# Kernel optimization log

Measured on AMD Instinct MI355X. Metric: run time of the kernel, lower is better.

The kernel has to match this reference:

```python
import jax, jax.numpy as jnp
import numpy as np

N_VERTEX = 50000
N_EDGE = 400000
HV, HE, P, Q, MV, ME = 128, 64, 3, 3, 128, 128


def setup_inputs() -> dict:
    key = jax.random.key(0)
    ks = jax.random.split(key, 12)
    hv_ftr = jax.random.normal(ks[0], (N_VERTEX, HV), jnp.float32)
    he_ftr = jax.random.normal(ks[1], (N_EDGE, HE), jnp.float32)
    p_ftr = jax.random.normal(ks[2], (N_VERTEX, P), jnp.float32)
    q_ftr = jax.random.normal(ks[3], (N_VERTEX, Q), jnp.float32)
    edge_u = jax.random.randint(ks[4], (N_EDGE,), 0, N_VERTEX, jnp.int32)
    edge_v = jax.random.randint(ks[5], (N_EDGE,), 0, N_VERTEX, jnp.int32)
    # Linear params stored as [in, out] (y = x @ W + b), matching torch Linear math.
    Wa = jax.random.normal(ks[6], (HV, MV), jnp.float32) * 0.05      # attend
    ba = jnp.zeros((MV,), jnp.float32)
    Wal = jax.random.normal(ks[7], (P + Q + HE, 1), jnp.float32) * 0.05  # align
    bal = jnp.zeros((1,), jnp.float32)
    Wl = jax.random.normal(ks[8], (2 * HV + P + Q, ME), jnp.float32) * 0.05  # link
    bl = jnp.zeros((ME,), jnp.float32)
    return dict(hv_ftr=hv_ftr, he_ftr=he_ftr, p_ftr=p_ftr, q_ftr=q_ftr,
                edge_u=edge_u, edge_v=edge_v,
                Wa=Wa, ba=ba, Wal=Wal, bal=bal, Wl=Wl, bl=bl)


def reference(hv_ftr, he_ftr, p_ftr, q_ftr, edge_u, edge_v, Wa, ba, Wal, bal, Wl, bl):
    # dropout is p=0.0 (identity). The dense vew/veb matmuls in the torch code
    # are exactly gathers / a per-vertex (segment) softmax / scatter-adds.
    E = he_ftr.shape[0]
    N = hv_ftr.shape[0]
    # bidirectionalize: vew_u = cat([vew1, vew2]), vew_v = cat([vew2, vew1])
    u = jnp.concatenate([edge_u, edge_v])  # [2E] source of each directed edge
    v = jnp.concatenate([edge_v, edge_u])  # [2E] destination

    hv_u = hv_ftr[u]                       # vew_u.T @ hv_ftr
    hv_v = hv_ftr[v]                       # vew_v.T @ hv_ftr
    p_uv = p_ftr[v] - p_ftr[u]
    q_uv = q_ftr[v] - q_ftr[u]
    he2 = jnp.concatenate([he_ftr, he_ftr], axis=0)

    attend = jax.nn.leaky_relu(hv_v @ Wa + ba)                       # [2E, MV]
    scores = (jnp.concatenate([p_uv, q_uv, he2], axis=1) @ Wal + bal).reshape(-1)  # [2E]

    # per-destination-vertex softmax over incident directed edges
    # (equals dense softmax of vew_v @ diag(scores) + veb_v with -inf mask bias)
    smax = jax.lax.stop_gradient(jax.ops.segment_max(scores, v, num_segments=N))
    ex = jnp.exp(scores - smax[v])
    denom = jax.ops.segment_sum(ex, v, num_segments=N)
    align = ex / denom[v]                                            # [2E]

    mv_ftr = jax.nn.elu(jax.ops.segment_sum(align[:, None] * attend, v, num_segments=N))  # [N, MV]

    me2 = jnp.concatenate([hv_u, p_uv, q_uv, hv_v], axis=1) @ Wl + bl  # [2E, ME]
    me_ftr = jax.nn.leaky_relu(me2[:E] + me2[E:])                      # [E, ME]
    return mv_ftr, me_ftr
```

## Files before the change

### kernel.cpp

```cpp
#include <hip/hip_runtime.h>
#include <math.h>

typedef unsigned short u16;
typedef __attribute__((ext_vector_type(8))) short short8;
typedef __attribute__((ext_vector_type(4))) float f32x4;

__device__ __forceinline__ u16 f2b(float f) {
    unsigned u = __float_as_uint(f);
    u += 0x7fffu + ((u >> 16) & 1u);
    return (u16)(u >> 16);
}

__device__ __forceinline__ short8 cvt8(const f32x4* __restrict__ p) {
    f32x4 a = p[0], b = p[1];
    short8 r;
    r[0] = (short)f2b(a[0]); r[1] = (short)f2b(a[1]);
    r[2] = (short)f2b(a[2]); r[3] = (short)f2b(a[3]);
    r[4] = (short)f2b(b[0]); r[5] = (short)f2b(b[1]);
    r[6] = (short)f2b(b[2]); r[7] = (short)f2b(b[3]);
    return r;
}

__global__ void k_prep(const float* __restrict__ Wa, const float* __restrict__ Wl,
                       u16* __restrict__ WpT, u16* __restrict__ WaT)
{
    const int c = blockIdx.x;
    const int k = threadIdx.x;
    WaT[c * 128 + k] = f2b(Wa[k * 128 + c]);
    WpT[c * 128 + k] = f2b(Wl[k * 128 + c] + Wl[(134 + k) * 128 + c]);
}

__global__ void k_mark0(unsigned char* __restrict__ mark, int NV)
{
    int i = blockIdx.x * 256 + threadIdx.x;
    if (i < NV) mark[i] = 0;
}

__global__ void k_mark(const int* __restrict__ eu, const int* __restrict__ ev,
                       unsigned char* __restrict__ mark, int NE)
{
    int i = blockIdx.x * 256 + threadIdx.x;
    if (i < NE) { mark[eu[i]] = 1; mark[ev[i]] = 1; }
}

__global__ __launch_bounds__(256, 2) void k_mv(
    const float* __restrict__ hv, const u16* __restrict__ WT, const float* __restrict__ ba,
    const unsigned char* __restrict__ mark, float* __restrict__ out, int NV)
{
    const int lane = threadIdx.x & 63;
    const int wv   = threadIdx.x >> 6;
    const int m = lane & 15, q = lane >> 4;
    const int n0 = blockIdx.x * 64 + wv * 16;

    int nl = n0 + m; if (nl >= NV) nl = NV - 1;

    short8 a[4];
    {
        const f32x4* ap = (const f32x4*)(hv + (size_t)nl * 128 + q * 8);
        #pragma unroll
        for (int ks = 0; ks < 4; ++ks) a[ks] = cvt8(ap + ks * 8);
    }

    f32x4 acc[8];
    #pragma unroll
    for (int t = 0; t < 8; ++t) acc[t] = (f32x4){0.f, 0.f, 0.f, 0.f};

    #pragma unroll
    for (int ks = 0; ks < 4; ++ks) {
        #pragma unroll
        for (int t = 0; t < 8; ++t) {
            short8 b = *(const short8*)(WT + (size_t)(t * 16 + m) * 128 + ks * 32 + q * 8);
            acc[t] = __builtin_amdgcn_mfma_f32_16x16x32_bf16(a[ks], b, acc[t], 0, 0, 0);
        }
    }

    #pragma unroll
    for (int t = 0; t < 8; ++t) {
        const int col  = t * 16 + m;
        const float bias = ba[col];
        #pragma unroll
        for (int i = 0; i < 4; ++i) {
            const int row = n0 + q * 4 + i;
            if (row < NV) {
                float z = acc[t][i] + bias;
                float y = (z > 0.f) ? z : 0.01f * z;
                float r = (y > 0.f) ? y : (__expf(y) - 1.f);
                if (mark[row] == 0) r = 0.f;
                out[(size_t)row * 128 + col] = r;
            }
        }
    }
}

__global__ __launch_bounds__(256, 2) void k_me(
    const float* __restrict__ hv, const int* __restrict__ eu, const int* __restrict__ ev,
    const u16* __restrict__ WT, const float* __restrict__ bl, float* __restrict__ out, int NE)
{
    const int lane = threadIdx.x & 63;
    const int wv   = threadIdx.x >> 6;
    const int m = lane & 15, q = lane >> 4;
    const int e0 = blockIdx.x * 64 + wv * 16;

    int e = e0 + m; if (e >= NE) e = NE - 1;
    const int iu = eu[e];
    const int iv = ev[e];

    short8 au[4], av[4];
    {
        const f32x4* up = (const f32x4*)(hv + (size_t)iu * 128 + q * 8);
        const f32x4* vp = (const f32x4*)(hv + (size_t)iv * 128 + q * 8);
        #pragma unroll
        for (int ks = 0; ks < 4; ++ks) { au[ks] = cvt8(up + ks * 8); av[ks] = cvt8(vp + ks * 8); }
    }

    f32x4 acc[8];
    #pragma unroll
    for (int t = 0; t < 8; ++t) acc[t] = (f32x4){0.f, 0.f, 0.f, 0.f};

    #pragma unroll
    for (int ks = 0; ks < 4; ++ks) {
        short8 b[8];
        #pragma unroll
        for (int t = 0; t < 8; ++t)
            b[t] = *(const short8*)(WT + (size_t)(t * 16 + m) * 128 + ks * 32 + q * 8);
        #pragma unroll
        for (int t = 0; t < 8; ++t)
            acc[t] = __builtin_amdgcn_mfma_f32_16x16x32_bf16(au[ks], b[t], acc[t], 0, 0, 0);
        #pragma unroll
        for (int t = 0; t < 8; ++t)
            acc[t] = __builtin_amdgcn_mfma_f32_16x16x32_bf16(av[ks], b[t], acc[t], 0, 0, 0);
    }

    #pragma unroll
    for (int t = 0; t < 8; ++t) {
        const int col  = t * 16 + m;
        const float bias = 2.0f * bl[col];
        #pragma unroll
        for (int i = 0; i < 4; ++i) {
            const int row = e0 + q * 4 + i;
            if (row < NE) {
                float x = acc[t][i] + bias;
                x = (x > 0.f) ? x : 0.01f * x;
                out[(size_t)row * 128 + col] = x;
            }
        }
    }
}

extern "C" void kernel_launch(void* const* d_in, const int* in_sizes, int n_in,
                              void* d_out, int out_size, void* d_ws, size_t ws_size,
                              hipStream_t stream)
{
    const float* hv = (const float*)d_in[0];
    const int*   eu = (const int*)d_in[4];
    const int*   ev = (const int*)d_in[5];
    const float* Wa = (const float*)d_in[6];
    const float* ba = (const float*)d_in[7];
    const float* Wl = (const float*)d_in[10];
    const float* bl = (const float*)d_in[11];

    const int NV = in_sizes[0] / 128;
    const int NE = in_sizes[4];

    u16* WpT = (u16*)d_ws;
    u16* WaT = WpT + 128 * 128;
    unsigned char* mark = (unsigned char*)(WaT + 128 * 128);

    float* mv_out = (float*)d_out;
    float* me_out = mv_out + (size_t)NV * 128;

    k_prep <<<128, 128, 0, stream>>>(Wa, Wl, WpT, WaT);
    k_mark0<<<(NV + 255) / 256, 256, 0, stream>>>(mark, NV);
    k_mark <<<(NE + 255) / 256, 256, 0, stream>>>(eu, ev, mark, NE);
    k_mv   <<<(NV + 63) / 64, 256, 0, stream>>>(hv, WaT, ba, mark, mv_out, NV);
    k_me   <<<(NE + 63) / 64, 256, 0, stream>>>(hv, eu, ev, WpT, bl, me_out, NE);
}
```

Baseline: 450.3 us.

## Pre-convert hv to bf16 once, fuse prep kernels, merge edge/vertex GEMMs into one launch

Adds a prep pass that converts hv_ftr to a bf16 copy in workspace, so the edge kernel gathers half the bytes per endpoint and skips per-edge conversion. The mark-clearing and weight-transpose kernels are folded into that prep kernel. The vertex and edge GEMM kernels become one launch split by block index, and output stores are nontemporal. A fallback path stages the bf16 copy in the mv output buffer when workspace is too small, which relies on the edge launch finishing before the vertex launch overwrites that buffer; the extra conversion pass adds a full read and write of hv.

```diff
diff --git a/kernel.cpp b/kernel.cpp
--- a/kernel.cpp
+++ b/kernel.cpp
@@ -21,19 +21,25 @@
     return r;
 }
 
-__global__ void k_prep(const float* __restrict__ Wa, const float* __restrict__ Wl,
-                       u16* __restrict__ WpT, u16* __restrict__ WaT)
-{
-    const int c = blockIdx.x;
-    const int k = threadIdx.x;
-    WaT[c * 128 + k] = f2b(Wa[k * 128 + c]);
-    WpT[c * 128 + k] = f2b(Wl[k * 128 + c] + Wl[(134 + k) * 128 + c]);
-}
-
-__global__ void k_mark0(unsigned char* __restrict__ mark, int NV)
-{
-    int i = blockIdx.x * 256 + threadIdx.x;
-    if (i < NV) mark[i] = 0;
+__global__ __launch_bounds__(256) void k_prep(
+    const float* __restrict__ hv, const float* __restrict__ Wa, const float* __restrict__ Wl,
+    u16* __restrict__ hvb, u16* __restrict__ WpT, u16* __restrict__ WaT,
+    unsigned char* __restrict__ mark, int NV, int nbHV)
+{
+    if ((int)blockIdx.x < nbHV) {
+        size_t base = (size_t)blockIdx.x * 2048 + (size_t)threadIdx.x * 8;
+        if (base + 8 <= (size_t)NV * 128) {
+            short8 r = cvt8((const f32x4*)(hv + base));
+            *(short8*)(hvb + base) = r;
+        }
+        int r0 = (int)blockIdx.x * 16 + (int)threadIdx.x;
+        if (threadIdx.x < 16 && r0 < NV) mark[r0] = 0;
+    } else {
+        int c = ((int)blockIdx.x - nbHV) * 2 + ((int)threadIdx.x >> 7);
+        int k = threadIdx.x & 127;
+        WaT[c * 128 + k] = f2b(Wa[k * 128 + c]);
+        WpT[c * 128 + k] = f2b(Wl[k * 128 + c] + Wl[(134 + k) * 128 + c]);
+    }
 }
 
 __global__ void k_mark(const int* __restrict__ eu, const int* __restrict__ ev,
@@ -43,105 +49,104 @@
     if (i < NE) { mark[eu[i]] = 1; mark[ev[i]] = 1; }
 }
 
-__global__ __launch_bounds__(256, 2) void k_mv(
-    const float* __restrict__ hv, const u16* __restrict__ WT, const float* __restrict__ ba,
-    const unsigned char* __restrict__ mark, float* __restrict__ out, int NV)
+__global__ __launch_bounds__(256) void k_main(
+    const u16* __restrict__ hvb, const float* __restrict__ hv,
+    const int* __restrict__ eu, const int* __restrict__ ev,
+    const u16* __restrict__ WpT, const u16* __restrict__ WaT,
+    const float* __restrict__ bl, const float* __restrict__ ba,
+    const unsigned char* __restrict__ mark,
+    float* __restrict__ mv_out, float* __restrict__ me_out,
+    int NE, int NV, int nbE)
 {
     const int lane = threadIdx.x & 63;
     const int wv   = threadIdx.x >> 6;
     const int m = lane & 15, q = lane >> 4;
-    const int n0 = blockIdx.x * 64 + wv * 16;
-
-    int nl = n0 + m; if (nl >= NV) nl = NV - 1;
-
-    short8 a[4];
-    {
-        const f32x4* ap = (const f32x4*)(hv + (size_t)nl * 128 + q * 8);
-        #pragma unroll
-        for (int ks = 0; ks < 4; ++ks) a[ks] = cvt8(ap + ks * 8);
-    }
-
-    f32x4 acc[8];
-    #pragma unroll
-    for (int t = 0; t < 8; ++t) acc[t] = (f32x4){0.f, 0.f, 0.f, 0.f};
-
-    #pragma unroll
-    for (int ks = 0; ks < 4; ++ks) {
+
+    if ((int)blockIdx.x < nbE) {
+        const int e0 = blockIdx.x * 64 + wv * 16;
+        int e = e0 + m; if (e >= NE) e = NE - 1;
+        const int iu = eu[e];
+        const int iv = ev[e];
+
+        short8 au[4], av[4];
+        {
+            const short8* up = (const short8*)(hvb + (size_t)iu * 128 + q * 8);
+            const short8* vp = (const short8*)(hvb + (size_t)iv * 128 + q * 8);
+            #pragma unroll
+            for (int ks = 0; ks < 4; ++ks) { au[ks] = up[ks * 4]; av[ks] = vp[ks * 4]; }
+        }
+
+        f32x4 acc[8];
+        #pragma unroll
+        for (int t = 0; t < 8; ++t) acc[t] = (f32x4){0.f, 0.f, 0.f, 0.f};
+
+        #pragma unroll
+        for (int ks = 0; ks < 4; ++ks) {
+            short8 b[8];
+            #pragma unroll
+            for (int t = 0; t < 8; ++t)
+                b[t] = *(const short8*)(WpT + (size_t)(t * 16 + m) * 128 + ks * 32 + q * 8);
+            #pragma unroll
+            for (int t = 0; t < 8; ++t)
+                acc[t] = __builtin_amdgcn_mfma_f32_16x16x32_bf16(au[ks], b[t], acc[t], 0, 0, 0);
+            #pragma unroll
+            for (int t = 0; t < 8; ++t)
+                acc[t] = __builtin_amdgcn_mfma_f32_16x16x32_bf16(av[ks], b[t], acc[t], 0, 0, 0);
+        }
+
         #pragma unroll
         for (int t = 0; t < 8; ++t) {
-            short8 b = *(const short8*)(WT + (size_t)(t * 16 + m) * 128 + ks * 32 + q * 8);
-            acc[t] = __builtin_amdgcn_mfma_f32_16x16x32_bf16(a[ks], b, acc[t], 0, 0, 0);
-        }
-    }
-
-    #pragma unroll
-    for (int t = 0; t < 8; ++t) {
-        const int col  = t * 16 + m;
-        const float bias = ba[col];
-        #pragma unroll
-        for (int i = 0; i < 4; ++i) {
-            const int row = n0 + q * 4 + i;
-            if (row < NV) {
-                float z = acc[t][i] + bias;
-                float y = (z > 0.f) ? z : 0.01f * z;
-                float r = (y > 0.f) ? y : (__expf(y) - 1.f);
-                if (mark[row] == 0) r = 0.f;
-                out[(size_t)row * 128 + col] = r;
+            const int col  = t * 16 + m;
+            const float bias = 2.0f * bl[col];
+            #pragma unroll
+            for (int i = 0; i < 4; ++i) {
+                const int row = e0 + q * 4 + i;
+                if (row < NE) {
+                    float x = acc[t][i] + bias;
+                    x = (x > 0.f) ? x : 0.01f * x;
+                    __builtin_nontemporal_store(x, &me_out[(size_t)row * 128 + col]);
+                }
             }
         }
-    }
-}
-
-__global__ __launch_bounds__(256, 2) void k_me(
-    const float* __restrict__ hv, const int* __restrict__ eu, const int* __restrict__ ev,
-    const u16* __restrict__ WT, const float* __restrict__ bl, float* __restrict__ out, int NE)
-{
-    const int lane = threadIdx.x & 63;
-    const int wv   = threadIdx.x >> 6;
-    const int m = lane & 15, q = lane >> 4;
-    const int e0 = blockIdx.x * 64 + wv * 16;
-
-    int e = e0 + m; if (e >= NE) e = NE - 1;
-    const int iu = eu[e];
-    const int iv = ev[e];
-
-    short8 au[4], av[4];
-    {
-        const f32x4* up = (const f32x4*)(hv + (size_t)iu * 128 + q * 8);
-        const f32x4* vp = (const f32x4*)(hv + (size_t)iv * 128 + q * 8);
-        #pragma unroll
-        for (int ks = 0; ks < 4; ++ks) { au[ks] = cvt8(up + ks * 8); av[ks] = cvt8(vp + ks * 8); }
-    }
-
-    f32x4 acc[8];
-    #pragma unroll
-    for (int t = 0; t < 8; ++t) acc[t] = (f32x4){0.f, 0.f, 0.f, 0.f};
-
-    #pragma unroll
-    for (int ks = 0; ks < 4; ++ks) {
-        short8 b[8];
-        #pragma unroll
-        for (int t = 0; t < 8; ++t)
-            b[t] = *(const short8*)(WT + (size_t)(t * 16 + m) * 128 + ks * 32 + q * 8);
-        #pragma unroll
-        for (int t = 0; t < 8; ++t)
-            acc[t] = __builtin_amdgcn_mfma_f32_16x16x32_bf16(au[ks], b[t], acc[t], 0, 0, 0);
-        #pragma unroll
-        for (int t = 0; t < 8; ++t)
-            acc[t] = __builtin_amdgcn_mfma_f32_16x16x32_bf16(av[ks], b[t], acc[t], 0, 0, 0);
-    }
-
-    #pragma unroll
-    for (int t = 0; t < 8; ++t) {
-        const int col  = t * 16 + m;
-        const float bias = 2.0f * bl[col];
-        #pragma unroll
-        for (int i = 0; i < 4; ++i) {
-            const int row = e0 + q * 4 + i;
-            if (row < NE) {
-                float x = acc[t][i] + bias;
-                x = (x > 0.f) ? x : 0.01f * x;
-                out[(size_t)row * 128 + col] = x;
+    } else {
+        const int vb = (int)blockIdx.x - nbE;
+        const int n0 = vb * 64 + wv * 16;
+        int nl = n0 + m; if (nl >= NV) nl = NV - 1;
+
+        short8 a[4];
+        {
+            const f32x4* ap = (const f32x4*)(hv + (size_t)nl * 128 + q * 8);
+            #pragma unroll
+            for (int ks = 0; ks < 4; ++ks) a[ks] = cvt8(ap + ks * 8);
+        }
+
+        f32x4 acc[8];
+        #pragma unroll
+        for (int t = 0; t < 8; ++t) acc[t] = (f32x4){0.f, 0.f, 0.f, 0.f};
+
+        #pragma unroll
+        for (int ks = 0; ks < 4; ++ks) {
+            #pragma unroll
+            for (int t = 0; t < 8; ++t) {
+                short8 b = *(const short8*)(WaT + (size_t)(t * 16 + m) * 128 + ks * 32 + q * 8);
+                acc[t] = __builtin_amdgcn_mfma_f32_16x16x32_bf16(a[ks], b, acc[t], 0, 0, 0);
+            }
+        }
+
+        #pragma unroll
+        for (int t = 0; t < 8; ++t) {
+            const int col  = t * 16 + m;
+            const float bias = ba[col];
+            #pragma unroll
+            for (int i = 0; i < 4; ++i) {
+                const int row = n0 + q * 4 + i;
+                if (row < NV) {
+                    float z = acc[t][i] + bias;
+                    float y = (z > 0.f) ? z : 0.01f * z;
+                    float r = (y > 0.f) ? y : (__expf(y) - 1.f);
+                    if (mark[row] == 0) r = 0.f;
+                    __builtin_nontemporal_store(r, &mv_out[(size_t)row * 128 + col]);
+                }
             }
         }
     }
@@ -162,16 +167,37 @@
     const int NV = in_sizes[0] / 128;
     const int NE = in_sizes[4];
 
-    u16* WpT = (u16*)d_ws;
-    u16* WaT = WpT + 128 * 128;
-    unsigned char* mark = (unsigned char*)(WaT + 128 * 128);
-
     float* mv_out = (float*)d_out;
     float* me_out = mv_out + (size_t)NV * 128;
 
-    k_prep <<<128, 128, 0, stream>>>(Wa, Wl, WpT, WaT);
-    k_mark0<<<(NV + 255) / 256, 256, 0, stream>>>(mark, NV);
-    k_mark <<<(NE + 255) / 256, 256, 0, stream>>>(eu, ev, mark, NE);
-    k_mv   <<<(NV + 63) / 64, 256, 0, stream>>>(hv, WaT, ba, mark, mv_out, NV);
-    k_me   <<<(NE + 63) / 64, 256, 0, stream>>>(hv, eu, ev, WpT, bl, me_out, NE);
-}
+    const int nbHV = (NV * 128 + 2047) / 2048;
+    const int nbE  = (NE + 63) / 64;
+    const int nbV  = (NV + 63) / 64;
+
+    const size_t hvb_bytes = (size_t)NV * 128 * 2;
+    const size_t need_ws   = hvb_bytes + 128 * 128 * 2 * 2 + (size_t)NV;
+
+    if (ws_size >= need_ws) {
+        u16* hvb = (u16*)d_ws;
+        u16* WpT = hvb + (size_t)NV * 128;
+        u16* WaT = WpT + 128 * 128;
+        unsigned char* mark = (unsigned char*)(WaT + 128 * 128);
+
+        k_prep<<<nbHV + 64, 256, 0, stream>>>(hv, Wa, Wl, hvb, WpT, WaT, mark, NV, nbHV);
+        k_mark<<<(NE + 255) / 256, 256, 0, stream>>>(eu, ev, mark, NE);
+        k_main<<<nbE + nbV, 256, 0, stream>>>(hvb, hv, eu, ev, WpT, WaT, bl, ba, mark,
+                                              mv_out, me_out, NE, NV, nbE);
+    } else {
+        u16* hvb = (u16*)mv_out;
+        u16* WpT = (u16*)d_ws;
+        u16* WaT = WpT + 128 * 128;
+        unsigned char* mark = (unsigned char*)(WaT + 128 * 128);
+
+        k_prep<<<nbHV + 64, 256, 0, stream>>>(hv, Wa, Wl, hvb, WpT, WaT, mark, NV, nbHV);
+        k_mark<<<(NE + 255) / 256, 256, 0, stream>>>(eu, ev, mark, NE);
+        k_main<<<nbE, 256, 0, stream>>>(hvb, hv, eu, ev, WpT, WaT, bl, ba, mark,
+                                        mv_out, me_out, NE, NV, nbE);
+        k_main<<<nbV, 256, 0, stream>>>(hvb, hv, eu, ev, WpT, WaT, bl, ba, mark,
+                                        mv_out, me_out, NE, NV, 0);
+    }
+}
```

New measurement: 428.8 us. -4.8%, faster.
